# Optimization experiments

Measured on AMD Instinct MI355X. Metric: run time of the kernel, lower is better.

## Reference

```python
import jax, jax.numpy as jnp
import numpy as np

B, S, D, H = 2, 2048, 1024, 16
DH = D // H  # 64


def setup_inputs() -> dict:
    key = jax.random.key(0)
    ks = jax.random.split(key, 10)
    inp = {
        "q": jax.random.normal(ks[0], (B, S, D), jnp.float32),
        "k": jax.random.normal(ks[1], (B, S, D), jnp.float32),
        "v": jax.random.normal(ks[2], (B, S, D), jnp.float32),
        "mask": jax.random.randint(ks[3], (B, S), 0, 2, jnp.int32),
        "Wq": jax.random.normal(ks[4], (D, D), jnp.float32) * 0.02,
        "bq": jnp.zeros((D,), jnp.float32),
        "Wk": jax.random.normal(ks[5], (D, D), jnp.float32) * 0.02,
        "bk": jnp.zeros((D,), jnp.float32),
        "Wv": jax.random.normal(ks[6], (D, D), jnp.float32) * 0.02,
        "bv": jnp.zeros((D,), jnp.float32),
    }
    return inp


def _split_heads(x):
    # [B, S, D] -> [B, H, S, DH]
    b, s, _ = x.shape
    return x.reshape(b, s, H, DH).transpose(0, 2, 1, 3)


def reference(q, k, v, mask, Wq, bq, Wk, bk, Wv, bv):
    qh = _split_heads(q @ Wq + bq)
    kh = _split_heads(k @ Wk + bk)
    vh = _split_heads(v @ Wv + bv)
    # NOTE: original scales by sqrt(hidden_size), not sqrt(head_dim)
    scores = jnp.einsum("bhqd,bhkd->bhqk", qh, kh) / jnp.sqrt(jnp.float32(D))
    m = mask.astype(jnp.float32)[:, None, None, :]  # [B,1,1,S_k]
    scores = scores + (-1e9) * (1.0 - m)
    weights = jax.nn.softmax(scores, axis=-1)
    out = jnp.einsum("bhqk,bhkd->bhqd", weights, vh)
    # concat heads: [B,H,S,DH] -> [B,S,D]
    return out.transpose(0, 2, 1, 3).reshape(q.shape[0], -1, D)
```

## Files before the change

### kernel.cpp

```cpp
#include <hip/hip_runtime.h>


#define B_ 2
#define S_ 2048
#define D_ 1024
#define H_ 16
#define DH_ 64
#define M_ (B_*S_)

#define WT_OFF  ((size_t)3*4194304)
#define XB_OFF  (WT_OFF + (size_t)3*1048576)

typedef __attribute__((ext_vector_type(8))) short short8;
typedef __attribute__((ext_vector_type(4))) float f32x4;
typedef __attribute__((ext_vector_type(4))) unsigned int u32x4;
#define MFMA16(a,b,c) __builtin_amdgcn_mfma_f32_16x16x32_bf16(a,b,c,0,0,0)

typedef __attribute__((address_space(1))) const void* gptr_t;
typedef __attribute__((address_space(3))) void* lptr_t;
static __device__ inline void gload_lds16(const void* g, void* l) {
    __builtin_amdgcn_global_load_lds((gptr_t)g, (lptr_t)l, 16, 0, 0);
}

static __device__ inline unsigned short f2bf(float x) {
    union { float f; unsigned u; } v; v.f = x;
    return (unsigned short)((v.u + 0x7fffu + ((v.u >> 16) & 1u)) >> 16);
}
static __device__ inline unsigned packp(float a, float b) {
    return __builtin_amdgcn_perm(__float_as_uint(b) + 0x8000u,
                                 __float_as_uint(a) + 0x8000u, 0x07060302u);
}

__global__ __launch_bounds__(256) void convert_all(
    const float* __restrict__ X0, const float* __restrict__ X1,
    const float* __restrict__ X2,
    const float* __restrict__ Wq, const float* __restrict__ Wk,
    const float* __restrict__ Wv,
    unsigned short* __restrict__ O0, unsigned short* __restrict__ O1,
    unsigned short* __restrict__ O2, unsigned short* __restrict__ WtBase)
{
    __shared__ unsigned short T[64][72];
    const int z = blockIdx.z;
    const int t = threadIdx.x;

    if (blockIdx.x < 4096) {
        const float* X = z==0 ? X0 : (z==1 ? X1 : X2);
        unsigned short* O = z==0 ? O0 : (z==1 ? O1 : O2);
        int idx = blockIdx.x*256 + t;
        float4 xv = *(const float4*)&X[(size_t)idx*4];
        uint2 o;
        o.x = (unsigned)f2bf(xv.x) | ((unsigned)f2bf(xv.y) << 16);
        o.y = (unsigned)f2bf(xv.z) | ((unsigned)f2bf(xv.w) << 16);
        *(uint2*)&O[(size_t)idx*4] = o;
        return;
    }

    const float* W = z==0 ? Wq : (z==1 ? Wk : Wv);
    unsigned short* Out = WtBase + ((size_t)z << 20);
    const int bx2 = blockIdx.x - 4096;
    const int n0 = (bx2 & 15)*64, k0 = (bx2 >> 4)*64;
    const int tk = t >> 4, tn4 = (t & 15)*4;

    #pragma unroll
    for (int i=0;i<4;i++){
        int kk = tk + i*16;
        float4 wv = *(const float4*)&W[(size_t)(k0+kk)*D_ + n0 + tn4];
        T[tn4+0][kk] = f2bf(wv.x);
        T[tn4+1][kk] = f2bf(wv.y);
        T[tn4+2][kk] = f2bf(wv.z);
        T[tn4+3][kk] = f2bf(wv.w);
    }
    __syncthreads();

    const int n = t >> 2, seg = t & 3;
    uint4 a = *(uint4*)&T[n][seg*16];
    uint4 b = *(uint4*)&T[n][seg*16 + 8];
    *(uint4*)&Out[(size_t)(n0+n)*D_ + k0 + seg*16]     = a;
    *(uint4*)&Out[(size_t)(n0+n)*D_ + k0 + seg*16 + 8] = b;
}

__global__ __launch_bounds__(256) void proj_gemm(
    const unsigned short* __restrict__ A0, const unsigned short* __restrict__ A1,
    const unsigned short* __restrict__ A2, const unsigned short* __restrict__ WtBase,
    const float* __restrict__ b0, const float* __restrict__ b1,
    const float* __restrict__ b2, unsigned short* __restrict__ OutBase)
{
    const int which = blockIdx.z;
    const unsigned short* A  = which==0 ? A0 : (which==1 ? A1 : A2);
    const unsigned short* Bm = WtBase + ((size_t)which << 20);
    const float* bias        = which==0 ? b0 : (which==1 ? b1 : b2);
    unsigned short* Out      = OutBase + ((size_t)which << 22);
    const float oscale = (which==0) ? 0.04508422f : 1.0f;

    __shared__ __align__(16) unsigned short As[128*64];
    __shared__ __align__(16) unsigned short Bs[128*64];

    const int t    = threadIdx.x;
    const int m0   = blockIdx.y * 128;
    const int n0   = blockIdx.x * 128;
    const int w    = t >> 6;
    const int lane = t & 63;
    const int l15  = lane & 15;
    const int quad = lane >> 4;
    const int wm   = w >> 1, wn = w & 1;

    f32x4 acc[4][4];
    #pragma unroll
    for (int i=0;i<4;i++)
        #pragma unroll
        for (int j=0;j<4;j++) acc[i][j] = (f32x4){0.f,0.f,0.f,0.f};

    float biasv[4];
    #pragma unroll
    for (int nt=0; nt<4; nt++)
        biasv[nt] = bias[n0 + wn*64 + nt*16 + l15];

    int sArow[4], sAkc[4];
    #pragma unroll
    for (int i=0;i<4;i++){
        int s  = (w*4 + i)*64 + lane;
        int r  = s >> 3, cs = s & 7;
        sArow[i] = r;
        sAkc[i]  = ((cs ^ (r & 7)) * 8);
    }

    for (int ks = 0; ks < 16; ++ks) {
        const int kb = ks * 64;
        #pragma unroll
        for (int i=0;i<4;i++){
            int s = (w*4 + i)*64 + lane;
            gload_lds16(A  + (size_t)(m0 + sArow[i])*D_ + kb + sAkc[i], (unsigned short*)As + s*8);
            gload_lds16(Bm + (size_t)(n0 + sArow[i])*D_ + kb + sAkc[i], (unsigned short*)Bs + s*8);
        }
        __syncthreads();

        #pragma unroll
        for (int kh=0; kh<2; kh++){
            short8 aF[4], bF[4];
            #pragma unroll
            for (int mt=0; mt<4; mt++){
                int r  = wm*64 + mt*16 + l15;
                int cs = (kh*4 + quad) ^ (r & 7);
                aF[mt] = *(const short8*)(As + r*64 + cs*8);
            }
            #pragma unroll
            for (int nt=0; nt<4; nt++){
                int r  = wn*64 + nt*16 + l15;
                int cs = (kh*4 + quad) ^ (r & 7);
                bF[nt] = *(const short8*)(Bs + r*64 + cs*8);
            }
            #pragma unroll
            for (int mt=0; mt<4; mt++)
                #pragma unroll
                for (int nt=0; nt<4; nt++)
                    acc[mt][nt] = MFMA16(aF[mt], bF[nt], acc[mt][nt]);
        }
        __syncthreads();
    }

    if (which != 2) {
        #pragma unroll
        for (int nt=0; nt<4; nt++){
            int n  = n0 + wn*64 + nt*16 + l15;
            int hh = n >> 6, dh = n & 63;
            #pragma unroll
            for (int mt=0; mt<4; mt++){
                #pragma unroll
                for (int r=0; r<4; r++){
                    int m  = m0 + wm*64 + mt*16 + quad*4 + r;
                    int bb = m >> 11, ss = m & (S_-1);
                    float v = (acc[mt][nt][r] + biasv[nt]) * oscale;
                    Out[((size_t)((bb*H_ + hh)*S_ + ss))*DH_ + dh] = f2bf(v);
                }
            }
        }
    } else {
        #pragma unroll
        for (int nt=0; nt<4; nt++){
            int n  = n0 + wn*64 + nt*16 + l15;
            int hh = n >> 6, dh = n & 63;
            #pragma unroll
            for (int mt=0; mt<4; mt++){
                int m  = m0 + wm*64 + mt*16 + quad*4;
                int bb = m >> 11, ss = m & (S_-1);
                uint2 pk;
                pk.x = packp(acc[mt][nt][0] + biasv[nt], acc[mt][nt][1] + biasv[nt]);
                pk.y = packp(acc[mt][nt][2] + biasv[nt], acc[mt][nt][3] + biasv[nt]);
                *(uint2*)&Out[((size_t)((bb*H_ + hh)*DH_ + dh))*S_ + ss] = pk;
            }
        }
    }
}

__global__ __launch_bounds__(256, 2) void attn_kernel(
    const unsigned short* __restrict__ ws, const int* __restrict__ mask,
    float* __restrict__ out)
{
    const unsigned short* Qh = ws;
    const unsigned short* Kh = ws + (size_t)M_*D_;
    const unsigned short* Vg = ws + 2*(size_t)M_*D_;

    const int lin = blockIdx.x + (blockIdx.y << 4) + (blockIdx.z << 8);
    const int Wn  = (lin & 7)*64 + (lin >> 3);
    const int qt = Wn & 15;
    const int h  = (Wn >> 4) & 15;
    const int bb = Wn >> 8;

    const size_t base = ((size_t)(bb*H_ + h)) * S_ * DH_;
    const int q0 = qt * 128;

    __shared__ __align__(16) unsigned char smem[73728];
    unsigned short* KsB = (unsigned short*)smem;
    unsigned short* VtB = (unsigned short*)(smem + 32768);
    float*          MsT = (float*)(smem + 65536);
    float*          Ob  = (float*)smem;

    const int t    = threadIdx.x;
    const int w    = t >> 6;
    const int lane = t & 63;
    const int l15  = lane & 15;
    const int quad = lane >> 4;

    short8 qf[2][2];
    #pragma unroll
    for (int qs=0; qs<2; qs++){
        const unsigned short* qp = Qh + base + (size_t)(q0 + w*32 + qs*16 + l15)*DH_ + quad*8;
        qf[qs][0] = *(const short8*)(qp);
        qf[qs][1] = *(const short8*)(qp + 32);
    }

    f32x4 accO[2][4];
    #pragma unroll
    for (int qs=0; qs<2; qs++)
        #pragma unroll
        for (int i=0;i<4;i++) accO[qs][i] = (f32x4){0.f,0.f,0.f,0.f};
    f32x4 lv[2] = {(f32x4){0.f,0.f,0.f,0.f}, (f32x4){0.f,0.f,0.f,0.f}};

    int rr[4], cc[4], ssl[4], gK[4];
    #pragma unroll
    for (int i=0;i<4;i++){
        int s  = (w*4 + i)*64 + lane;
        int r  = s >> 3, cs = s & 7;
        int r6 = r & 63;
        ssl[i] = s;
        rr[i]  = r;
        cc[i]  = (cs ^ (r & 7)) * 8;
        gK[i]  = (r & 64) + ((r6 >> 4) & 1)*32 + ((r6 >> 2) & 3)*8 + (r6 >> 5)*4 + (r6 & 3);
    }

    #define ISSUE128(k0v, p) do {                                              \
        _Pragma("unroll")                                                      \
        for (int i=0;i<4;i++){                                                 \
            gload_lds16(Kh + base + (size_t)((k0v) + gK[i])*DH_ + cc[i],       \
                        KsB + (p)*8192 + ssl[i]*8);                            \
            gload_lds16(Vg + base + (size_t)(rr[i] & 63)*S_ + (k0v)            \
                            + (rr[i] & 64) + cc[i],                            \
                        VtB + (p)*8192 + ssl[i]*8);                            \
        }                                                                      \
    } while(0)

    ISSUE128(0, 0);
    #pragma unroll
    for (int i=0;i<8;i++){
        int idx = i*256 + t;
        MsT[idx] = mask[bb*S_ + idx] ? 0.f : -1e9f;
    }
    __syncthreads();

    for (int it = 0; it < 16; ++it){
        const int p = it & 1;
        if (it < 15) ISSUE128((it+1)*128, 1-p);

        #pragma unroll
        for (int sb = 0; sb < 2; ++sb){
            const unsigned short* Ks  = KsB + p*8192 + sb*4096;
            const unsigned short* Vts = VtB + p*8192 + sb*4096;
            const float*          Mp  = MsT + it*128 + sb*64;

            f32x4 msv[4];
            #pragma unroll
            for (int st=0; st<4; st++)
                msv[st] = *(const f32x4*)&Mp[(st&1)*32 + (st>>1)*4 + quad*8];

            short8 ka[4], kb[4];
            #pragma unroll
            for (int st=0; st<4; st++){
                int row = st*16 + l15;
                const unsigned short* kr = Ks + row*64;
                ka[st] = *(const short8*)(kr + ((quad    ) ^ (row & 7))*8);
                kb[st] = *(const short8*)(kr + ((quad + 4) ^ (row & 7))*8);
            }
            short8 vf[4][2];
            #pragma unroll
            for (int mt=0; mt<4; mt++){
                int row = mt*16 + l15;
                const unsigned short* vr = Vts + row*64;
                vf[mt][0] = *(const short8*)(vr + ((quad    ) ^ (row & 7))*8);
                vf[mt][1] = *(const short8*)(vr + ((quad + 4) ^ (row & 7))*8);
            }

            #pragma unroll
            for (int qs=0; qs<2; qs++){
                f32x4 sc[4];
                __builtin_amdgcn_s_setprio(1);
                #pragma unroll
                for (int st=0; st<4; st++){
                    f32x4 a = msv[st];
                    a = MFMA16(ka[st], qf[qs][0], a);
                    a = MFMA16(kb[st], qf[qs][1], a);
                    sc[st] = a;
                }
                __builtin_amdgcn_s_setprio(0);
                f32x4 pvv[4];
                #pragma unroll
                for (int st=0; st<4; st++)
                    #pragma unroll
                    for (int rj=0; rj<4; rj++)
                        pvv[st][rj] = __builtin_amdgcn_exp2f(sc[st][rj]);
                f32x4 s01 = pvv[0] + pvv[1];
                f32x4 s23 = pvv[2] + pvv[3];
                lv[qs] += (s01 + s23);
                u32x4 u0 = { packp(pvv[0][0],pvv[0][1]), packp(pvv[0][2],pvv[0][3]),
                             packp(pvv[2][0],pvv[2][1]), packp(pvv[2][2],pvv[2][3]) };
                u32x4 u1 = { packp(pvv[1][0],pvv[1][1]), packp(pvv[1][2],pvv[1][3]),
                             packp(pvv[3][0],pvv[3][1]), packp(pvv[3][2],pvv[3][3]) };
                short8 pf0 = __builtin_bit_cast(short8, u0);
                short8 pf1 = __builtin_bit_cast(short8, u1);
                __builtin_amdgcn_s_setprio(1);
                #pragma unroll
                for (int mt=0; mt<4; mt++){
                    accO[qs][mt] = MFMA16(vf[mt][0], pf0, accO[qs][mt]);
                    accO[qs][mt] = MFMA16(vf[mt][1], pf1, accO[qs][mt]);
                }
                __builtin_amdgcn_s_setprio(0);
            }
        }
        __syncthreads();
    }

    #pragma unroll
    for (int qs=0; qs<2; qs++){
        float l = (lv[qs][0] + lv[qs][1]) + (lv[qs][2] + lv[qs][3]);
        l += __shfl_xor(l, 16);
        l += __shfl_xor(l, 32);
        float invl = 1.0f / fmaxf(l, 1e-30f);
        #pragma unroll
        for (int mt=0; mt<4; mt++)
            #pragma unroll
            for (int r=0; r<4; r++)
                Ob[(w*32 + qs*16 + l15)*68 + mt*16 + quad*4 + r] = accO[qs][mt][r]*invl;
    }
    __syncthreads();

    #pragma unroll
    for (int i=0;i<8;i++){
        int f  = (i*256 + t)*4;
        int qq = f >> 6, dh = f & 63;
        float4 o = *(float4*)&Ob[qq*68 + dh];
        *(float4*)&out[((size_t)(bb*S_ + q0 + qq))*D_ + h*DH_ + dh] = o;
    }
    #undef ISSUE128
}

extern "C" void kernel_launch(void* const* d_in, const int* in_sizes, int n_in,
                              void* d_out, int out_size, void* d_ws, size_t ws_size,
                              hipStream_t stream) {
    const float* q    = (const float*)d_in[0];
    const float* k    = (const float*)d_in[1];
    const float* v    = (const float*)d_in[2];
    const int*   mask = (const int*)d_in[3];
    const float* Wq   = (const float*)d_in[4];
    const float* b0   = (const float*)d_in[5];
    const float* Wk   = (const float*)d_in[6];
    const float* b1   = (const float*)d_in[7];
    const float* Wv   = (const float*)d_in[8];
    const float* b2   = (const float*)d_in[9];
    float* out = (float*)d_out;
    unsigned short* ws = (unsigned short*)d_ws;

    unsigned short* xq = ws + XB_OFF;
    unsigned short* xk = (unsigned short*)d_out;
    unsigned short* xv = (unsigned short*)d_out + 4194304;

    convert_all<<<dim3(4352,1,3), 256, 0, stream>>>(q, k, v, Wq, Wk, Wv,
                                                    xq, xk, xv, ws + WT_OFF);
    proj_gemm<<<dim3(8,32,3), 256, 0, stream>>>(xq, xk, xv, ws + WT_OFF,
                                                b0, b1, b2, ws);
    attn_kernel<<<dim3(16,16,2), 256, 0, stream>>>(ws, mask, out);
}
```

Measured before the change: 202.2 us.

## Split attention key tiles across wave pairs and swizzle projection GEMM block order

The attention kernel moves from 256 to 512 threads. Each pair of waves shares the same 32 query rows and takes one half of every 128-key tile, so per-wave MFMA work per iteration is halved and more waves are available to hide latency. The two partial output accumulators and row sums are combined through LDS at the end before normalisation. The projection GEMM also remaps its block indices with a swizzle so that neighbouring blocks land on different M/N tiles and matrices, which is meant to improve cache locality. The tighter launch bound (512, 4) caps registers per thread and could cause spills, and the cross-wave reduction adds extra LDS traffic and a sync.

```diff
diff --git a/kernel.cpp b/kernel.cpp
--- a/kernel.cpp
+++ b/kernel.cpp
@@ -85,7 +85,12 @@
     const float* __restrict__ b0, const float* __restrict__ b1,
     const float* __restrict__ b2, unsigned short* __restrict__ OutBase)
 {
-    const int which = blockIdx.z;
+    const int lin0 = blockIdx.x + (blockIdx.y << 3) + (blockIdx.z << 8);
+    const int swz  = (lin0 & 7)*96 + (lin0 >> 3);
+    const int bxn  = swz & 7;
+    const int byn  = (swz >> 3) & 31;
+    const int which = swz >> 8;
+
     const unsigned short* A  = which==0 ? A0 : (which==1 ? A1 : A2);
     const unsigned short* Bm = WtBase + ((size_t)which << 20);
     const float* bias        = which==0 ? b0 : (which==1 ? b1 : b2);
@@ -96,8 +101,8 @@
     __shared__ __align__(16) unsigned short Bs[128*64];
 
     const int t    = threadIdx.x;
-    const int m0   = blockIdx.y * 128;
-    const int n0   = blockIdx.x * 128;
+    const int m0   = byn * 128;
+    const int n0   = bxn * 128;
     const int w    = t >> 6;
     const int lane = t & 63;
     const int l15  = lane & 15;
@@ -192,7 +197,7 @@
     }
 }
 
-__global__ __launch_bounds__(256, 2) void attn_kernel(
+__global__ __launch_bounds__(512, 4) void attn_kernel(
     const unsigned short* __restrict__ ws, const int* __restrict__ mask,
     float* __restrict__ out)
 {
@@ -214,17 +219,21 @@
     unsigned short* VtB = (unsigned short*)(smem + 32768);
     float*          MsT = (float*)(smem + 65536);
     float*          Ob  = (float*)smem;
+    float*          Lb  = (float*)(smem + 36864);
+    float*          invL= (float*)(smem + 38912);
 
     const int t    = threadIdx.x;
     const int w    = t >> 6;
     const int lane = t & 63;
     const int l15  = lane & 15;
     const int quad = lane >> 4;
+    const int qw   = w >> 1;
+    const int pb   = w & 1;
 
     short8 qf[2][2];
     #pragma unroll
     for (int qs=0; qs<2; qs++){
-        const unsigned short* qp = Qh + base + (size_t)(q0 + w*32 + qs*16 + l15)*DH_ + quad*8;
+        const unsigned short* qp = Qh + base + (size_t)(q0 + qw*32 + qs*16 + l15)*DH_ + quad*8;
         qf[qs][0] = *(const short8*)(qp);
         qf[qs][1] = *(const short8*)(qp + 32);
     }
@@ -236,10 +245,10 @@
         for (int i=0;i<4;i++) accO[qs][i] = (f32x4){0.f,0.f,0.f,0.f};
     f32x4 lv[2] = {(f32x4){0.f,0.f,0.f,0.f}, (f32x4){0.f,0.f,0.f,0.f}};
 
-    int rr[4], cc[4], ssl[4], gK[4];
-    #pragma unroll
-    for (int i=0;i<4;i++){
-        int s  = (w*4 + i)*64 + lane;
+    int rr[2], cc[2], ssl[2], gK[2];
+    #pragma unroll
+    for (int i=0;i<2;i++){
+        int s  = (w*2 + i)*64 + lane;
         int r  = s >> 3, cs = s & 7;
         int r6 = r & 63;
         ssl[i] = s;
@@ -250,7 +259,7 @@
 
     #define ISSUE128(k0v, p) do {                                              \
         _Pragma("unroll")                                                      \
-        for (int i=0;i<4;i++){                                                 \
+        for (int i=0;i<2;i++){                                                 \
             gload_lds16(Kh + base + (size_t)((k0v) + gK[i])*DH_ + cc[i],       \
                         KsB + (p)*8192 + ssl[i]*8);                            \
             gload_lds16(Vg + base + (size_t)(rr[i] & 63)*S_ + (k0v)            \
@@ -261,8 +270,8 @@
 
     ISSUE128(0, 0);
     #pragma unroll
-    for (int i=0;i<8;i++){
-        int idx = i*256 + t;
+    for (int i=0;i<4;i++){
+        int idx = i*512 + t;
         MsT[idx] = mask[bb*S_ + idx] ? 0.f : -1e9f;
     }
     __syncthreads();
@@ -271,92 +280,112 @@
         const int p = it & 1;
         if (it < 15) ISSUE128((it+1)*128, 1-p);
 
-        #pragma unroll
-        for (int sb = 0; sb < 2; ++sb){
-            const unsigned short* Ks  = KsB + p*8192 + sb*4096;
-            const unsigned short* Vts = VtB + p*8192 + sb*4096;
-            const float*          Mp  = MsT + it*128 + sb*64;
-
-            f32x4 msv[4];
+        const unsigned short* Ks  = KsB + p*8192 + pb*4096;
+        const unsigned short* Vts = VtB + p*8192 + pb*4096;
+        const float*          Mp  = MsT + it*128 + pb*64;
+
+        f32x4 msv[4];
+        #pragma unroll
+        for (int st=0; st<4; st++)
+            msv[st] = *(const f32x4*)&Mp[(st&1)*32 + (st>>1)*4 + quad*8];
+
+        short8 ka[4], kb[4];
+        #pragma unroll
+        for (int st=0; st<4; st++){
+            int row = st*16 + l15;
+            const unsigned short* kr = Ks + row*64;
+            ka[st] = *(const short8*)(kr + ((quad    ) ^ (row & 7))*8);
+            kb[st] = *(const short8*)(kr + ((quad + 4) ^ (row & 7))*8);
+        }
+        short8 vf[4][2];
+        #pragma unroll
+        for (int mt=0; mt<4; mt++){
+            int row = mt*16 + l15;
+            const unsigned short* vr = Vts + row*64;
+            vf[mt][0] = *(const short8*)(vr + ((quad    ) ^ (row & 7))*8);
+            vf[mt][1] = *(const short8*)(vr + ((quad + 4) ^ (row & 7))*8);
+        }
+
+        #pragma unroll
+        for (int qs=0; qs<2; qs++){
+            f32x4 sc[4];
+            __builtin_amdgcn_s_setprio(1);
+            #pragma unroll
+            for (int st=0; st<4; st++){
+                f32x4 a = msv[st];
+                a = MFMA16(ka[st], qf[qs][0], a);
+                a = MFMA16(kb[st], qf[qs][1], a);
+                sc[st] = a;
+            }
+            __builtin_amdgcn_s_setprio(0);
+            f32x4 pvv[4];
             #pragma unroll
             for (int st=0; st<4; st++)
-                msv[st] = *(const f32x4*)&Mp[(st&1)*32 + (st>>1)*4 + quad*8];
-
-            short8 ka[4], kb[4];
-            #pragma unroll
-            for (int st=0; st<4; st++){
-                int row = st*16 + l15;
-                const unsigned short* kr = Ks + row*64;
-                ka[st] = *(const short8*)(kr + ((quad    ) ^ (row & 7))*8);
-                kb[st] = *(const short8*)(kr + ((quad + 4) ^ (row & 7))*8);
-            }
-            short8 vf[4][2];
+                #pragma unroll
+                for (int rj=0; rj<4; rj++)
+                    pvv[st][rj] = __builtin_amdgcn_exp2f(sc[st][rj]);
+            f32x4 s01 = pvv[0] + pvv[1];
+            f32x4 s23 = pvv[2] + pvv[3];
+            lv[qs] += (s01 + s23);
+            u32x4 u0 = { packp(pvv[0][0],pvv[0][1]), packp(pvv[0][2],pvv[0][3]),
+                         packp(pvv[2][0],pvv[2][1]), packp(pvv[2][2],pvv[2][3]) };
+            u32x4 u1 = { packp(pvv[1][0],pvv[1][1]), packp(pvv[1][2],pvv[1][3]),
+                         packp(pvv[3][0],pvv[3][1]), packp(pvv[3][2],pvv[3][3]) };
+            short8 pf0 = __builtin_bit_cast(short8, u0);
+            short8 pf1 = __builtin_bit_cast(short8, u1);
+            __builtin_amdgcn_s_setprio(1);
             #pragma unroll
             for (int mt=0; mt<4; mt++){
-                int row = mt*16 + l15;
-                const unsigned short* vr = Vts + row*64;
-                vf[mt][0] = *(const short8*)(vr + ((quad    ) ^ (row & 7))*8);
-                vf[mt][1] = *(const short8*)(vr + ((quad + 4) ^ (row & 7))*8);
-            }
-
-            #pragma unroll
-            for (int qs=0; qs<2; qs++){
-                f32x4 sc[4];
-                __builtin_amdgcn_s_setprio(1);
-                #pragma unroll
-                for (int st=0; st<4; st++){
-                    f32x4 a = msv[st];
-                    a = MFMA16(ka[st], qf[qs][0], a);
-                    a = MFMA16(kb[st], qf[qs][1], a);
-                    sc[st] = a;
-                }
-                __builtin_amdgcn_s_setprio(0);
-                f32x4 pvv[4];
-                #pragma unroll
-                for (int st=0; st<4; st++)
-                    #pragma unroll
-                    for (int rj=0; rj<4; rj++)
-                        pvv[st][rj] = __builtin_amdgcn_exp2f(sc[st][rj]);
-                f32x4 s01 = pvv[0] + pvv[1];
-                f32x4 s23 = pvv[2] + pvv[3];
-                lv[qs] += (s01 + s23);
-                u32x4 u0 = { packp(pvv[0][0],pvv[0][1]), packp(pvv[0][2],pvv[0][3]),
-                             packp(pvv[2][0],pvv[2][1]), packp(pvv[2][2],pvv[2][3]) };
-                u32x4 u1 = { packp(pvv[1][0],pvv[1][1]), packp(pvv[1][2],pvv[1][3]),
-                             packp(pvv[3][0],pvv[3][1]), packp(pvv[3][2],pvv[3][3]) };
-                short8 pf0 = __builtin_bit_cast(short8, u0);
-                short8 pf1 = __builtin_bit_cast(short8, u1);
-                __builtin_amdgcn_s_setprio(1);
-                #pragma unroll
-                for (int mt=0; mt<4; mt++){
-                    accO[qs][mt] = MFMA16(vf[mt][0], pf0, accO[qs][mt]);
-                    accO[qs][mt] = MFMA16(vf[mt][1], pf1, accO[qs][mt]);
-                }
-                __builtin_amdgcn_s_setprio(0);
-            }
+                accO[qs][mt] = MFMA16(vf[mt][0], pf0, accO[qs][mt]);
+                accO[qs][mt] = MFMA16(vf[mt][1], pf1, accO[qs][mt]);
+            }
+            __builtin_amdgcn_s_setprio(0);
         }
         __syncthreads();
     }
 
+    float lpart[2];
     #pragma unroll
     for (int qs=0; qs<2; qs++){
         float l = (lv[qs][0] + lv[qs][1]) + (lv[qs][2] + lv[qs][3]);
         l += __shfl_xor(l, 16);
         l += __shfl_xor(l, 32);
-        float invl = 1.0f / fmaxf(l, 1e-30f);
-        #pragma unroll
-        for (int mt=0; mt<4; mt++)
-            #pragma unroll
-            for (int r=0; r<4; r++)
-                Ob[(w*32 + qs*16 + l15)*68 + mt*16 + quad*4 + r] = accO[qs][mt][r]*invl;
+        lpart[qs] = l;
+    }
+    if (quad == 0){
+        #pragma unroll
+        for (int qs=0; qs<2; qs++)
+            Lb[pb*128 + qw*32 + qs*16 + l15] = lpart[qs];
+    }
+    if (pb == 0){
+        #pragma unroll
+        for (int qs=0; qs<2; qs++)
+            #pragma unroll
+            for (int mt=0; mt<4; mt++)
+                #pragma unroll
+                for (int r=0; r<4; r++)
+                    Ob[(qw*32 + qs*16 + l15)*68 + mt*16 + quad*4 + r] = accO[qs][mt][r];
     }
     __syncthreads();
-
-    #pragma unroll
-    for (int i=0;i<8;i++){
-        int f  = (i*256 + t)*4;
+    if (pb == 1){
+        #pragma unroll
+        for (int qs=0; qs<2; qs++)
+            #pragma unroll
+            for (int mt=0; mt<4; mt++)
+                #pragma unroll
+                for (int r=0; r<4; r++)
+                    Ob[(qw*32 + qs*16 + l15)*68 + mt*16 + quad*4 + r] += accO[qs][mt][r];
+    }
+    if (t < 128) invL[t] = 1.0f / fmaxf(Lb[t] + Lb[128 + t], 1e-30f);
+    __syncthreads();
+
+    #pragma unroll
+    for (int i=0;i<4;i++){
+        int f  = (i*512 + t)*4;
         int qq = f >> 6, dh = f & 63;
         float4 o = *(float4*)&Ob[qq*68 + dh];
+        float s = invL[qq];
+        o.x *= s; o.y *= s; o.z *= s; o.w *= s;
         *(float4*)&out[((size_t)(bb*S_ + q0 + qq))*D_ + h*DH_ + dh] = o;
     }
     #undef ISSUE128
@@ -386,5 +415,5 @@
                                                     xq, xk, xv, ws + WT_OFF);
     proj_gemm<<<dim3(8,32,3), 256, 0, stream>>>(xq, xk, xv, ws + WT_OFF,
                                                 b0, b1, b2, ws);
-    attn_kernel<<<dim3(16,16,2), 256, 0, stream>>>(ws, mask, out);
-}
+    attn_kernel<<<dim3(16,16,2), 512, 0, stream>>>(ws, mask, out);
+}
```

Result: slower. 363.0 us (+79.6%).
